# Optimization experiments

Hardware: AMD Instinct MI355X
Metric: run time of the kernel (lower is better)

## Reference

```python
import jax, jax.numpy as jnp
import numpy as np

S, H, A = 8192, 4096, 1024

def setup_inputs() -> dict:
    key = jax.random.key(0)
    ks = jax.random.split(key, 8)
    return {
        "encoder_outputs": jax.random.normal(ks[0], (S, H), jnp.float32),
        "hidden": jax.random.normal(ks[1], (H,), jnp.float32),
        "U_w": jax.random.normal(ks[2], (A, H), jnp.float32) * (1.0 / np.sqrt(H)),
        "U_b": jax.random.normal(ks[3], (A,), jnp.float32) * 0.01,
        "W_w": jax.random.normal(ks[4], (A, H), jnp.float32) * (1.0 / np.sqrt(H)),
        "W_b": jax.random.normal(ks[5], (A,), jnp.float32) * 0.01,
        "V_w": jax.random.normal(ks[6], (1, A), jnp.float32) * (1.0 / np.sqrt(A)),
        "V_b": jax.random.normal(ks[7], (1,), jnp.float32) * 0.01,
    }

def reference(encoder_outputs, hidden, U_w, U_b, W_w, W_b, V_w, V_b):
    # Bahdanau additive attention ('add' mode).
    W_hidden = hidden @ W_w.T + W_b                      # [A]
    U_encode = encoder_outputs @ U_w.T + U_b             # [S, A]
    poly_tanh = jnp.tanh(U_encode + W_hidden)            # [S, A]
    scores = poly_tanh @ V_w.T + V_b                     # [S, 1]
    attn = jax.nn.softmax(scores, axis=0)                # softmax over sequence
    context = attn.T @ encoder_outputs                   # [1, H]
    return context[None]                                 # [1, 1, H] (matches torch bmm)
```

## Files before the change

kernel.cpp:

```cpp
#include <hip/hip_runtime.h>

typedef __attribute__((ext_vector_type(8))) short short8;
typedef __attribute__((ext_vector_type(4))) float f32x4;

#define S_DIM 8192
#define H_DIM 4096
#define A_DIM 1024

__device__ __forceinline__ short f2bf(float x) {
  unsigned u = __float_as_uint(x);
  u += 0x7fffu + ((u >> 16) & 1u);
  return (short)(u >> 16);
}

__device__ __forceinline__ float bf2f(short b) {
  return __uint_as_float(((unsigned)(unsigned short)b) << 16);
}

__device__ __forceinline__ void gload16(const void* g, void* l) {
  __builtin_amdgcn_global_load_lds(
      (const __attribute__((address_space(1))) void*)g,
      (__attribute__((address_space(3))) void*)l, 16, 0, 0);
}

__global__ __launch_bounds__(256) void comb_kernel(const float* __restrict__ hidden,
                                                   const float* __restrict__ Ww,
                                                   const float* __restrict__ Wb,
                                                   const float* __restrict__ Ub,
                                                   float* __restrict__ comb) {
  const int wave = threadIdx.x >> 6;
  const int lane = threadIdx.x & 63;
  const int a = blockIdx.x * 4 + wave;
  const float* row = Ww + (size_t)a * H_DIM;
  float acc = 0.f;
  for (int k = lane * 4; k < H_DIM; k += 64 * 4) {
    float4 w = *(const float4*)(row + k);
    float4 h = *(const float4*)(hidden + k);
    acc += w.x * h.x + w.y * h.y + w.z * h.z + w.w * h.w;
  }
  #pragma unroll
  for (int mk = 1; mk < 64; mk <<= 1) acc += __shfl_xor(acc, mk);
  if (lane == 0) comb[a] = acc + Wb[a] + Ub[a];
}

__global__ __launch_bounds__(256) void cvt_kernel(const float* __restrict__ src,
                                                  unsigned short* __restrict__ dst,
                                                  int n8) {
  const int stride = gridDim.x * blockDim.x;
  for (int i = blockIdx.x * blockDim.x + threadIdx.x; i < n8; i += stride) {
    float4 a = ((const float4*)src)[(size_t)i * 2];
    float4 b = ((const float4*)src)[(size_t)i * 2 + 1];
    short8 o;
    o[0] = f2bf(a.x); o[1] = f2bf(a.y); o[2] = f2bf(a.z); o[3] = f2bf(a.w);
    o[4] = f2bf(b.x); o[5] = f2bf(b.y); o[6] = f2bf(b.z); o[7] = f2bf(b.w);
    ((short8*)dst)[i] = o;
  }
}

__global__ __launch_bounds__(256) void gemm_kspl_kernel(
    const unsigned short* __restrict__ A,
    const unsigned short* __restrict__ B,
    float* __restrict__ partialC) {
  __shared__ __align__(16) unsigned short sA[128 * 64];
  __shared__ __align__(16) unsigned short sB[128 * 64];

  const int tid  = threadIdx.x;
  const int lane = tid & 63;
  const int wave = tid >> 6;
  const int wm = wave >> 1, wn = wave & 1;
  const int m0 = blockIdx.x * 128;
  const int n0 = blockIdx.y * 128;
  const int k0 = blockIdx.z * (H_DIM / 2);

  const int srow = wave * 32 + (lane >> 3);
  const int scol = (lane & 7) * 8;
  const unsigned short* ga = A + (size_t)(m0 + srow) * H_DIM + k0 + scol;
  const unsigned short* gb = B + (size_t)(n0 + srow) * H_DIM + k0 + scol;

  #define STAGE(kt) do {                                                     \
    const unsigned short* pa_ = ga + (size_t)(kt) * 64;                      \
    const unsigned short* pb_ = gb + (size_t)(kt) * 64;                      \
    _Pragma("unroll")                                                        \
    for (int i_ = 0; i_ < 4; ++i_) {                                         \
      gload16(pa_ + (size_t)i_ * 8 * H_DIM, &sA[(wave * 4 + i_) * 512]);     \
      gload16(pb_ + (size_t)i_ * 8 * H_DIM, &sB[(wave * 4 + i_) * 512]);     \
    }                                                                        \
  } while (0)

  f32x4 acc[4][4];
  const f32x4 zero = {0.f, 0.f, 0.f, 0.f};
  #pragma unroll
  for (int i = 0; i < 4; ++i)
    #pragma unroll
    for (int j = 0; j < 4; ++j) acc[i][j] = zero;

  STAGE(0);

  const int NK = (H_DIM / 2) / 64;
  for (int kt = 0; kt < NK; ++kt) {
    __syncthreads();

    short8 af[2][4], bfr[2][4];
    #pragma unroll
    for (int ks = 0; ks < 2; ++ks) {
      #pragma unroll
      for (int i = 0; i < 4; ++i)
        af[ks][i] = *(const short8*)&sA[(wm * 64 + i * 16 + (lane & 15)) * 64 + ks * 32 + (lane >> 4) * 8];
      #pragma unroll
      for (int j = 0; j < 4; ++j)
        bfr[ks][j] = *(const short8*)&sB[(wn * 64 + j * 16 + (lane & 15)) * 64 + ks * 32 + (lane >> 4) * 8];
    }
    __syncthreads();

    if (kt + 1 < NK) STAGE(kt + 1);

    #pragma unroll
    for (int ks = 0; ks < 2; ++ks)
      #pragma unroll
      for (int i = 0; i < 4; ++i)
        #pragma unroll
        for (int j = 0; j < 4; ++j)
          acc[i][j] = __builtin_amdgcn_mfma_f32_16x16x32_bf16(af[ks][i], bfr[ks][j], acc[ks ? i : i][j], 0, 0, 0);
  }
  #undef STAGE

  float* pc = partialC + (size_t)blockIdx.z * S_DIM * A_DIM;
  #pragma unroll
  for (int i = 0; i < 4; ++i) {
    #pragma unroll
    for (int r = 0; r < 4; ++r) {
      const int grow = m0 + wm * 64 + i * 16 + (lane >> 4) * 4 + r;
      float* prow = pc + (size_t)grow * A_DIM + n0 + wn * 64 + (lane & 15);
      #pragma unroll
      for (int j = 0; j < 4; ++j) prow[j * 16] = acc[i][j][r];
    }
  }
}

__global__ __launch_bounds__(256) void tanh_score_kernel(
    const float* __restrict__ P,
    const float* __restrict__ comb,
    const float* __restrict__ Vw,
    float* __restrict__ scores) {
  const int lane = threadIdx.x & 63;
  const int wave = threadIdx.x >> 6;
  float4 vw[4], cb[4];
  #pragma unroll
  for (int c = 0; c < 4; ++c) {
    vw[c] = *(const float4*)&Vw[c * 256 + lane * 4];
    cb[c] = *(const float4*)&comb[c * 256 + lane * 4];
  }
  const float* P1 = P + (size_t)S_DIM * A_DIM;
  const int row0 = (blockIdx.x * 4 + wave) * 4;
  #pragma unroll
  for (int rr = 0; rr < 4; ++rr) {
    const int s = row0 + rr;
    const float* p0 = P  + (size_t)s * A_DIM;
    const float* p1 = P1 + (size_t)s * A_DIM;
    float acc = 0.f;
    #pragma unroll
    for (int c = 0; c < 4; ++c) {
      float4 x0 = *(const float4*)&p0[c * 256 + lane * 4];
      float4 x1 = *(const float4*)&p1[c * 256 + lane * 4];
      acc += vw[c].x * tanhf(x0.x + x1.x + cb[c].x);
      acc += vw[c].y * tanhf(x0.y + x1.y + cb[c].y);
      acc += vw[c].z * tanhf(x0.z + x1.z + cb[c].z);
      acc += vw[c].w * tanhf(x0.w + x1.w + cb[c].w);
    }
    #pragma unroll
    for (int mk = 1; mk < 64; mk <<= 1) acc += __shfl_xor(acc, mk);
    if (lane == 0) scores[s] = acc;
  }
}

__global__ __launch_bounds__(1024) void softmax_kernel(const float* __restrict__ scores,
                                                       float* __restrict__ attn) {
  __shared__ float redm[16];
  __shared__ float reds[16];
  const int tid = threadIdx.x;
  const int lane = tid & 63, wid = tid >> 6;
  float v[8];
  float m = -3.0e38f;
  #pragma unroll
  for (int i = 0; i < 8; ++i) { v[i] = scores[i * 1024 + tid]; m = fmaxf(m, v[i]); }
  #pragma unroll
  for (int mk = 1; mk < 64; mk <<= 1) m = fmaxf(m, __shfl_xor(m, mk));
  if (lane == 0) redm[wid] = m;
  __syncthreads();
  float M = redm[0];
  #pragma unroll
  for (int j = 1; j < 16; ++j) M = fmaxf(M, redm[j]);
  float e[8]; float s = 0.f;
  #pragma unroll
  for (int i = 0; i < 8; ++i) { e[i] = __expf(v[i] - M); s += e[i]; }
  #pragma unroll
  for (int mk = 1; mk < 64; mk <<= 1) s += __shfl_xor(s, mk);
  if (lane == 0) reds[wid] = s;
  __syncthreads();
  float T = 0.f;
  #pragma unroll
  for (int j = 0; j < 16; ++j) T += reds[j];
  const float inv = 1.f / T;
  #pragma unroll
  for (int i = 0; i < 8; ++i) attn[i * 1024 + tid] = e[i] * inv;
}

__global__ __launch_bounds__(256) void context_bf_kernel(const unsigned short* __restrict__ Ebf,
                                                         const float* __restrict__ attn,
                                                         float* __restrict__ partial) {
  const int h0 = (blockIdx.x * 256 + threadIdx.x) * 8;
  const int s0 = blockIdx.y * 64;
  float acc[8] = {0.f, 0.f, 0.f, 0.f, 0.f, 0.f, 0.f, 0.f};
  for (int s = s0; s < s0 + 64; ++s) {
    const float w = attn[s];
    short8 e = *(const short8*)(Ebf + (size_t)s * H_DIM + h0);
    #pragma unroll
    for (int j = 0; j < 8; ++j) acc[j] += w * bf2f(e[j]);
  }
  float* p = partial + (size_t)blockIdx.y * H_DIM + h0;
  #pragma unroll
  for (int j = 0; j < 8; ++j) p[j] = acc[j];
}

__global__ __launch_bounds__(256) void context_reduce_kernel(const float* __restrict__ partial,
                                                             float* __restrict__ out) {
  const int h = blockIdx.x * 256 + threadIdx.x;
  float acc = 0.f;
  #pragma unroll 8
  for (int y = 0; y < 128; ++y) acc += partial[(size_t)y * H_DIM + h];
  out[h] = acc;
}


__global__ __launch_bounds__(256) void gemm_score_bf_kernel(
    const unsigned short* __restrict__ A,
    const unsigned short* __restrict__ B,
    const float* __restrict__ comb,
    const float* __restrict__ Vw,
    float* __restrict__ scores) {
  __shared__ __align__(16) unsigned short sA[128 * 64];
  __shared__ __align__(16) unsigned short sB[128 * 64];
  const int tid  = threadIdx.x;
  const int lane = tid & 63;
  const int wave = tid >> 6;
  const int wm = wave >> 1, wn = wave & 1;
  const int m0 = blockIdx.x * 128;
  const int n0 = blockIdx.y * 128;
  const int srow = wave * 32 + (lane >> 3);
  const int scol = (lane & 7) * 8;
  const unsigned short* ga = A + (size_t)(m0 + srow) * H_DIM + scol;
  const unsigned short* gb = B + (size_t)(n0 + srow) * H_DIM + scol;
  #define STAGE(kt) do {                                                     \
    const unsigned short* pa_ = ga + (size_t)(kt) * 64;                      \
    const unsigned short* pb_ = gb + (size_t)(kt) * 64;                      \
    _Pragma("unroll")                                                        \
    for (int i_ = 0; i_ < 4; ++i_) {                                         \
      gload16(pa_ + (size_t)i_ * 8 * H_DIM, &sA[(wave * 4 + i_) * 512]);     \
      gload16(pb_ + (size_t)i_ * 8 * H_DIM, &sB[(wave * 4 + i_) * 512]);     \
    }                                                                        \
  } while (0)
  f32x4 acc[4][4];
  const f32x4 zero = {0.f, 0.f, 0.f, 0.f};
  #pragma unroll
  for (int i = 0; i < 4; ++i)
    #pragma unroll
    for (int j = 0; j < 4; ++j) acc[i][j] = zero;
  STAGE(0);
  const int NK = H_DIM / 64;
  for (int kt = 0; kt < NK; ++kt) {
    __syncthreads();
    short8 af[2][4], bfr[2][4];
    #pragma unroll
    for (int ks = 0; ks < 2; ++ks) {
      #pragma unroll
      for (int i = 0; i < 4; ++i)
        af[ks][i] = *(const short8*)&sA[(wm * 64 + i * 16 + (lane & 15)) * 64 + ks * 32 + (lane >> 4) * 8];
      #pragma unroll
      for (int j = 0; j < 4; ++j)
        bfr[ks][j] = *(const short8*)&sB[(wn * 64 + j * 16 + (lane & 15)) * 64 + ks * 32 + (lane >> 4) * 8];
    }
    __syncthreads();
    if (kt + 1 < NK) STAGE(kt + 1);
    #pragma unroll
    for (int ks = 0; ks < 2; ++ks)
      #pragma unroll
      for (int i = 0; i < 4; ++i)
        #pragma unroll
        for (int j = 0; j < 4; ++j)
          acc[i][j] = __builtin_amdgcn_mfma_f32_16x16x32_bf16(af[ks][i], bfr[ks][j], acc[i][j], 0, 0, 0);
  }
  #undef STAGE
  float vwv[4], cbv[4];
  #pragma unroll
  for (int j = 0; j < 4; ++j) {
    const int col = n0 + wn * 64 + j * 16 + (lane & 15);
    vwv[j] = Vw[col];
    cbv[j] = comb[col];
  }
  #pragma unroll
  for (int i = 0; i < 4; ++i) {
    #pragma unroll
    for (int r = 0; r < 4; ++r) {
      float s = 0.f;
      #pragma unroll
      for (int j = 0; j < 4; ++j)
        s += vwv[j] * tanhf(acc[i][j][r] + cbv[j]);
      s += __shfl_xor(s, 1);
      s += __shfl_xor(s, 2);
      s += __shfl_xor(s, 4);
      s += __shfl_xor(s, 8);
      if ((lane & 15) == 0) {
        const int grow = m0 + wm * 64 + i * 16 + (lane >> 4) * 4 + r;
        atomicAdd(&scores[grow], s);
      }
    }
  }
}


extern "C" void kernel_launch(void* const* d_in, const int* in_sizes, int n_in,
                              void* d_out, int out_size, void* d_ws, size_t ws_size,
                              hipStream_t stream) {
  const float* E   = (const float*)d_in[0];
  const float* hid = (const float*)d_in[1];
  const float* Uw  = (const float*)d_in[2];
  const float* Ub  = (const float*)d_in[3];
  const float* Ww  = (const float*)d_in[4];
  const float* Wb  = (const float*)d_in[5];
  const float* Vw  = (const float*)d_in[6];

  float* out    = (float*)d_out;
  float* ws     = (float*)d_ws;
  float* comb   = ws;
  float* scores = ws + 1024;
  float* attn   = ws + 1024 + 8192;
  float* ctxp   = ws + 17408;
  const size_t CTXP = (size_t)128 * H_DIM;

  float* pC = ws + 17408 + CTXP;
  unsigned short* Ebf2  = (unsigned short*)(pC + 2 * (size_t)S_DIM * A_DIM);
  unsigned short* Uwbf2 = Ebf2 + (size_t)S_DIM * H_DIM;
  const size_t NEED2 = ((size_t)17408 + CTXP + 2 * (size_t)S_DIM * A_DIM) * 4
                     + ((size_t)S_DIM + A_DIM) * H_DIM * 2;

  unsigned short* Ebf1  = (unsigned short*)(ws + 17408 + CTXP);
  unsigned short* Uwbf1 = Ebf1 + (size_t)S_DIM * H_DIM;
  const size_t NEED1 = ((size_t)17408 + CTXP) * 4
                     + ((size_t)S_DIM + A_DIM) * H_DIM * 2;

  comb_kernel<<<A_DIM / 4, 256, 0, stream>>>(hid, Ww, Wb, Ub, comb);

  if (ws_size >= NEED2) {
    cvt_kernel<<<2048, 256, 0, stream>>>(E, Ebf2, (int)((size_t)S_DIM * H_DIM / 8));
    cvt_kernel<<<512, 256, 0, stream>>>(Uw, Uwbf2, (int)((size_t)A_DIM * H_DIM / 8));

    gemm_kspl_kernel<<<dim3(S_DIM / 128, A_DIM / 128, 2), 256, 0, stream>>>(Ebf2, Uwbf2, pC);
    tanh_score_kernel<<<512, 256, 0, stream>>>(pC, comb, Vw, scores);

    softmax_kernel<<<1, 1024, 0, stream>>>(scores, attn);

    context_bf_kernel<<<dim3(H_DIM / 2048, S_DIM / 64), 256, 0, stream>>>(Ebf2, attn, ctxp);
    context_reduce_kernel<<<H_DIM / 256, 256, 0, stream>>>(ctxp, out);
  } else {
    hipMemsetAsync(scores, 0, S_DIM * sizeof(float), stream);
    cvt_kernel<<<2048, 256, 0, stream>>>(E, Ebf1, (int)((size_t)S_DIM * H_DIM / 8));
    cvt_kernel<<<512, 256, 0, stream>>>(Uw, Uwbf1, (int)((size_t)A_DIM * H_DIM / 8));

    gemm_score_bf_kernel<<<dim3(S_DIM / 128, A_DIM / 128), 256, 0, stream>>>(Ebf1, Uwbf1, comb, Vw, scores);
    softmax_kernel<<<1, 1024, 0, stream>>>(scores, attn);
    context_bf_kernel<<<dim3(H_DIM / 2048, S_DIM / 64), 256, 0, stream>>>(Ebf1, attn, ctxp);
    context_reduce_kernel<<<H_DIM / 256, 256, 0, stream>>>(ctxp, out);
  }
}
```

Before: 172.8 us.

## Store split-K partial GEMM results in bf16 and use fast tanh

The split-K GEMM now writes its two partial products as bf16 instead of fp32, which halves the intermediate traffic between the GEMM and the tanh/score kernel. The score kernel is restructured to one row per wave with 16 contiguous bf16 elements per lane, and it launches more blocks. tanhf is replaced by an exp-based fast_tanh in both score paths. In exchange, rounding the partials to bf16 before summing and using the approximate tanh add numerical error to the attention scores.

```diff
diff --git a/kernel.cpp b/kernel.cpp
--- a/kernel.cpp
+++ b/kernel.cpp
@@ -15,6 +15,12 @@
 
 __device__ __forceinline__ float bf2f(short b) {
   return __uint_as_float(((unsigned)(unsigned short)b) << 16);
+}
+
+__device__ __forceinline__ float fast_tanh(float x) {
+  float e = __expf(-2.f * fabsf(x));
+  float r = __fdividef(1.f - e, 1.f + e);
+  return copysignf(r, x);
 }
 
 __device__ __forceinline__ void gload16(const void* g, void* l) {
@@ -60,7 +66,7 @@
 __global__ __launch_bounds__(256) void gemm_kspl_kernel(
     const unsigned short* __restrict__ A,
     const unsigned short* __restrict__ B,
-    float* __restrict__ partialC) {
+    unsigned short* __restrict__ partialC) {
   __shared__ __align__(16) unsigned short sA[128 * 64];
   __shared__ __align__(16) unsigned short sB[128 * 64];
 
@@ -120,57 +126,56 @@
       for (int i = 0; i < 4; ++i)
         #pragma unroll
         for (int j = 0; j < 4; ++j)
-          acc[i][j] = __builtin_amdgcn_mfma_f32_16x16x32_bf16(af[ks][i], bfr[ks][j], acc[ks ? i : i][j], 0, 0, 0);
+          acc[i][j] = __builtin_amdgcn_mfma_f32_16x16x32_bf16(af[ks][i], bfr[ks][j], acc[i][j], 0, 0, 0);
   }
   #undef STAGE
 
-  float* pc = partialC + (size_t)blockIdx.z * S_DIM * A_DIM;
+  unsigned short* pc = partialC + (size_t)blockIdx.z * S_DIM * A_DIM;
   #pragma unroll
   for (int i = 0; i < 4; ++i) {
     #pragma unroll
     for (int r = 0; r < 4; ++r) {
       const int grow = m0 + wm * 64 + i * 16 + (lane >> 4) * 4 + r;
-      float* prow = pc + (size_t)grow * A_DIM + n0 + wn * 64 + (lane & 15);
-      #pragma unroll
-      for (int j = 0; j < 4; ++j) prow[j * 16] = acc[i][j][r];
+      unsigned short* prow = pc + (size_t)grow * A_DIM + n0 + wn * 64 + (lane & 15);
+      #pragma unroll
+      for (int j = 0; j < 4; ++j) prow[j * 16] = (unsigned short)f2bf(acc[i][j][r]);
     }
   }
 }
 
 __global__ __launch_bounds__(256) void tanh_score_kernel(
-    const float* __restrict__ P,
+    const unsigned short* __restrict__ P,
     const float* __restrict__ comb,
     const float* __restrict__ Vw,
     float* __restrict__ scores) {
   const int lane = threadIdx.x & 63;
   const int wave = threadIdx.x >> 6;
-  float4 vw[4], cb[4];
+  const int s = blockIdx.x * 4 + wave;
+  const unsigned short* p0 = P + (size_t)s * A_DIM + lane * 16;
+  const unsigned short* p1 = p0 + (size_t)S_DIM * A_DIM;
+
+  short8 a0 = *(const short8*)(p0);
+  short8 a1 = *(const short8*)(p0 + 8);
+  short8 b0 = *(const short8*)(p1);
+  short8 b1 = *(const short8*)(p1 + 8);
+  float4 cb[4], vw[4];
   #pragma unroll
   for (int c = 0; c < 4; ++c) {
-    vw[c] = *(const float4*)&Vw[c * 256 + lane * 4];
-    cb[c] = *(const float4*)&comb[c * 256 + lane * 4];
-  }
-  const float* P1 = P + (size_t)S_DIM * A_DIM;
-  const int row0 = (blockIdx.x * 4 + wave) * 4;
-  #pragma unroll
-  for (int rr = 0; rr < 4; ++rr) {
-    const int s = row0 + rr;
-    const float* p0 = P  + (size_t)s * A_DIM;
-    const float* p1 = P1 + (size_t)s * A_DIM;
-    float acc = 0.f;
-    #pragma unroll
-    for (int c = 0; c < 4; ++c) {
-      float4 x0 = *(const float4*)&p0[c * 256 + lane * 4];
-      float4 x1 = *(const float4*)&p1[c * 256 + lane * 4];
-      acc += vw[c].x * tanhf(x0.x + x1.x + cb[c].x);
-      acc += vw[c].y * tanhf(x0.y + x1.y + cb[c].y);
-      acc += vw[c].z * tanhf(x0.z + x1.z + cb[c].z);
-      acc += vw[c].w * tanhf(x0.w + x1.w + cb[c].w);
-    }
-    #pragma unroll
-    for (int mk = 1; mk < 64; mk <<= 1) acc += __shfl_xor(acc, mk);
-    if (lane == 0) scores[s] = acc;
-  }
+    cb[c] = *(const float4*)(comb + lane * 16 + c * 4);
+    vw[c] = *(const float4*)(Vw + lane * 16 + c * 4);
+  }
+
+  float acc = 0.f;
+  #pragma unroll
+  for (int j = 0; j < 8; ++j) {
+    float x = bf2f(a0[j]) + bf2f(b0[j]) + ((const float*)cb)[j];
+    acc += ((const float*)vw)[j] * fast_tanh(x);
+    float y = bf2f(a1[j]) + bf2f(b1[j]) + ((const float*)cb)[8 + j];
+    acc += ((const float*)vw)[8 + j] * fast_tanh(y);
+  }
+  #pragma unroll
+  for (int mk = 1; mk < 64; mk <<= 1) acc += __shfl_xor(acc, mk);
+  if (lane == 0) scores[s] = acc;
 }
 
 __global__ __launch_bounds__(1024) void softmax_kernel(const float* __restrict__ scores,
@@ -304,7 +309,7 @@
       float s = 0.f;
       #pragma unroll
       for (int j = 0; j < 4; ++j)
-        s += vwv[j] * tanhf(acc[i][j][r] + cbv[j]);
+        s += vwv[j] * fast_tanh(acc[i][j][r] + cbv[j]);
       s += __shfl_xor(s, 1);
       s += __shfl_xor(s, 2);
       s += __shfl_xor(s, 4);
@@ -337,10 +342,11 @@
   float* ctxp   = ws + 17408;
   const size_t CTXP = (size_t)128 * H_DIM;
 
-  float* pC = ws + 17408 + CTXP;
-  unsigned short* Ebf2  = (unsigned short*)(pC + 2 * (size_t)S_DIM * A_DIM);
+  unsigned short* pC    = (unsigned short*)(ws + 17408 + CTXP);
+  unsigned short* Ebf2  = pC + 2 * (size_t)S_DIM * A_DIM;
   unsigned short* Uwbf2 = Ebf2 + (size_t)S_DIM * H_DIM;
-  const size_t NEED2 = ((size_t)17408 + CTXP + 2 * (size_t)S_DIM * A_DIM) * 4
+  const size_t NEED2 = ((size_t)17408 + CTXP) * 4
+                     + 2 * (size_t)S_DIM * A_DIM * 2
                      + ((size_t)S_DIM + A_DIM) * H_DIM * 2;
 
   unsigned short* Ebf1  = (unsigned short*)(ws + 17408 + CTXP);
@@ -355,7 +361,7 @@
     cvt_kernel<<<512, 256, 0, stream>>>(Uw, Uwbf2, (int)((size_t)A_DIM * H_DIM / 8));
 
     gemm_kspl_kernel<<<dim3(S_DIM / 128, A_DIM / 128, 2), 256, 0, stream>>>(Ebf2, Uwbf2, pC);
-    tanh_score_kernel<<<512, 256, 0, stream>>>(pC, comb, Vw, scores);
+    tanh_score_kernel<<<S_DIM / 4, 256, 0, stream>>>(pC, comb, Vw, scores);
 
     softmax_kernel<<<1, 1024, 0, stream>>>(scores, attn);
 
```

Result: faster. 164.2 us (-5.0%).
